# Kernel tuning notes

Hardware: AMD Instinct MI355X
Metric: run time of the kernel (lower is better)

## Reference

```python
import jax, jax.numpy as jnp
import numpy as np

B, L, C, D = 32, 256, 16, 128
WORD_VOCAB, CHR_VOCAB = 50000, 128


def conv1d(x, w, b):
    # x: [N, D, T], w: [D_out, D_in, 3], torch Conv1d (cross-correlation), padding=1
    y = jax.lax.conv_general_dilated(x, w, window_strides=(1,), padding=[(1, 1)],
                                     dimension_numbers=('NCH', 'OIH', 'NCH'))
    return y + b[None, :, None]


def setup_inputs() -> dict:
    key = jax.random.key(0)
    k1, k2, k3, k4, k5, k6, k7, k8 = jax.random.split(key, 8)
    word_vector = jax.random.randint(k1, (B, L), 0, WORD_VOCAB)
    words_in_char = jax.random.randint(k2, (B, L, C), 0, CHR_VOCAB)
    # embedding tables, padding_idx=0 -> row 0 is zeros
    word_table = (jax.random.normal(k3, (WORD_VOCAB, D), jnp.float32) * 0.02).at[0].set(0.0)
    chr_table = (jax.random.normal(k4, (CHR_VOCAB, D), jnp.float32) * 0.02).at[0].set(0.0)
    scale = 1.0 / np.sqrt(D * 3)
    conv_chr_w = jax.random.normal(k5, (D, D, 3), jnp.float32) * scale
    conv_chr_b = jax.random.normal(k6, (D,), jnp.float32) * scale
    conv_word_w = jax.random.normal(k7, (D, D, 3), jnp.float32) * scale
    conv_word_b = jax.random.normal(k8, (D,), jnp.float32) * scale
    return dict(word_vector=word_vector, words_in_char=words_in_char,
                word_table=word_table, chr_table=chr_table,
                conv_chr_w=conv_chr_w, conv_chr_b=conv_chr_b,
                conv_word_w=conv_word_w, conv_word_b=conv_word_b)


def reference(word_vector, words_in_char, word_table, chr_table,
              conv_chr_w, conv_chr_b, conv_word_w, conv_word_b):
    # --- char path (batched version of the per-word Python loop) ---
    chr_emb = chr_table[words_in_char]                       # [B, L, C, D]
    x = chr_emb.reshape(B * L, C, D).transpose(0, 2, 1)      # [B*L, D, C]
    word_conv = conv1d(x, conv_chr_w, conv_chr_b)            # [B*L, D, C]
    char_feats = word_conv.max(axis=2).reshape(B, L, D)      # max over char positions
    # --- word path ---
    word_emb = word_table[word_vector]                       # [B, L, D]
    out = conv1d(word_emb.transpose(0, 2, 1), conv_word_w, conv_word_b)  # [B, D, L]
    # stack both branch outputs into one array: [2, B, D, L]
    return jnp.stack([out, char_feats.transpose(0, 2, 1)])
```

## Files before the change

kernel.cpp:

```cpp
#include <hip/hip_runtime.h>

typedef __attribute__((ext_vector_type(8))) short short8;
typedef __attribute__((ext_vector_type(4))) float float4_t;

#define NB 32
#define NL 256
#define ND 128
#define OUT_PLANE (NB * ND * NL)
#define XS 136

__device__ inline unsigned short f2bf(float f) {
    union { float f; unsigned int i; } c;
    c.f = f;
    unsigned int r = c.i + 0x7FFFu + ((c.i >> 16) & 1u);
    return (unsigned short)(r >> 16);
}

__global__ void make_frags(const float* __restrict__ Wc,
                           const float* __restrict__ Ww,
                           unsigned short* __restrict__ out) {
    int i = blockIdx.x * 256 + threadIdx.x;
    const int half = 12 * 8 * 64 * 8;
    const float* W = (i < half) ? Wc : Ww;
    int ii = (i < half) ? i : i - half;
    int j    = ii & 7;
    int lane = (ii >> 3) & 63;
    int nt   = (ii >> 9) & 7;
    int s    = ii >> 12;
    int dout = nt * 16 + (lane & 15);
    int t    = s >> 2;
    int k    = (s & 3) * 32 + ((lane >> 4) & 3) * 8 + j;
    out[i] = f2bf(W[(dout * 128 + k) * 3 + t]);
}

__global__ __launch_bounds__(128, 2) void conv_kernel(
    const int* __restrict__ wv, const int* __restrict__ wic,
    const float* __restrict__ wordT, const float* __restrict__ chrT,
    const unsigned short* __restrict__ frags,
    const float* __restrict__ biasC, const float* __restrict__ biasW,
    float* __restrict__ out) {
    __shared__ unsigned short X[2][18 * XS];
    const int tid  = threadIdx.x;
    const int wave = tid >> 6, lane = tid & 63;
    const int m = lane & 15, quad = lane >> 4;
    const int bid = blockIdx.x;

    if (bid >= 512) {
        const int w0 = (bid - 512) * 8;
        short8 bfrag[12][4];
#pragma unroll
        for (int s = 0; s < 12; ++s)
#pragma unroll
            for (int p = 0; p < 4; ++p)
                bfrag[s][p] = *(const short8*)(
                    frags + (((s * 8 + wave * 4 + p) * 64 + lane) << 3));
        float bb[4];
#pragma unroll
        for (int p = 0; p < 4; ++p) bb[p] = biasC[wave * 64 + p * 16 + m];

        for (int p = tid; p < XS; p += 128) {
            X[0][p] = 0; X[0][17 * XS + p] = 0;
            X[1][p] = 0; X[1][17 * XS + p] = 0;
        }
        const int r = tid >> 3, seg = tid & 7;

        {
            int idx0 = wic[w0 * 16 + r];
            const float4_t* src = (const float4_t*)(chrT + idx0 * 128 + seg * 16);
            float4_t f0 = src[0], f1 = src[1], f2 = src[2], f3 = src[3];
            unsigned short t16[16];
            t16[0]=f2bf(f0.x); t16[1]=f2bf(f0.y); t16[2]=f2bf(f0.z); t16[3]=f2bf(f0.w);
            t16[4]=f2bf(f1.x); t16[5]=f2bf(f1.y); t16[6]=f2bf(f1.z); t16[7]=f2bf(f1.w);
            t16[8]=f2bf(f2.x); t16[9]=f2bf(f2.y); t16[10]=f2bf(f2.z); t16[11]=f2bf(f2.w);
            t16[12]=f2bf(f3.x); t16[13]=f2bf(f3.y); t16[14]=f2bf(f3.z); t16[15]=f2bf(f3.w);
            *(short8*)&X[0][(r + 1) * XS + seg * 16]     = *(const short8*)&t16[0];
            *(short8*)&X[0][(r + 1) * XS + seg * 16 + 8] = *(const short8*)&t16[8];
        }
        int idxA = wic[(w0 + 1) * 16 + r];
        __syncthreads();

#pragma unroll
        for (int wl = 0; wl < 8; ++wl) {
            const int cur = wl & 1;
            float4_t f0, f1, f2, f3;
            if (wl < 7) {
                const float4_t* src =
                    (const float4_t*)(chrT + idxA * 128 + seg * 16);
                f0 = src[0]; f1 = src[1]; f2 = src[2]; f3 = src[3];
            }
            int idxB = (wl < 6) ? wic[(w0 + wl + 2) * 16 + r] : 0;

            float4_t acc[4];
#pragma unroll
            for (int p = 0; p < 4; ++p) acc[p] = (float4_t){0.f, 0.f, 0.f, 0.f};
#pragma unroll
            for (int s = 0; s < 12; ++s) {
                short8 a = *(const short8*)&X[cur][(m + (s >> 2)) * XS +
                                                  (s & 3) * 32 + quad * 8];
#pragma unroll
                for (int p = 0; p < 4; ++p)
                    acc[p] = __builtin_amdgcn_mfma_f32_16x16x32_bf16(
                        a, bfrag[s][p], acc[p], 0, 0, 0);
            }

            if (wl < 7) {
                unsigned short t16[16];
                t16[0]=f2bf(f0.x); t16[1]=f2bf(f0.y); t16[2]=f2bf(f0.z); t16[3]=f2bf(f0.w);
                t16[4]=f2bf(f1.x); t16[5]=f2bf(f1.y); t16[6]=f2bf(f1.z); t16[7]=f2bf(f1.w);
                t16[8]=f2bf(f2.x); t16[9]=f2bf(f2.y); t16[10]=f2bf(f2.z); t16[11]=f2bf(f2.w);
                t16[12]=f2bf(f3.x); t16[13]=f2bf(f3.y); t16[14]=f2bf(f3.z); t16[15]=f2bf(f3.w);
                *(short8*)&X[cur ^ 1][(r + 1) * XS + seg * 16]     = *(const short8*)&t16[0];
                *(short8*)&X[cur ^ 1][(r + 1) * XS + seg * 16 + 8] = *(const short8*)&t16[8];
                idxA = idxB;
            }
            __syncthreads();

            int w = w0 + wl, b = w >> 8, l = w & 255;
            float* obase = out + OUT_PLANE + b * (ND * NL) + l;
#pragma unroll
            for (int p = 0; p < 4; ++p) {
                float v = fmaxf(fmaxf(acc[p].x, acc[p].y),
                                fmaxf(acc[p].z, acc[p].w));
                v = fmaxf(v, __shfl_xor(v, 16, 64));
                v = fmaxf(v, __shfl_xor(v, 32, 64));
                v += bb[p];
                if (quad == 0) obase[(wave * 64 + p * 16 + m) * NL] = v;
            }
        }
    } else {
        const int b = bid >> 4, l0 = (bid & 15) << 4;
        short8 bfrag[12][4];
#pragma unroll
        for (int s = 0; s < 12; ++s)
#pragma unroll
            for (int p = 0; p < 4; ++p)
                bfrag[s][p] = *(const short8*)(
                    frags + 49152 + (((s * 8 + wave * 4 + p) * 64 + lane) << 3));
        float bb[4];
#pragma unroll
        for (int p = 0; p < 4; ++p) bb[p] = biasW[wave * 64 + p * 16 + m];

#pragma unroll
        for (int i0 = 0; i0 < 2; ++i0) {
            int i = tid + i0 * 128;
            if (i < 144) {
                int rr = i >> 3, sg = i & 7;
                int l = l0 + rr - 1;
                int idx = (l >= 0 && l < NL) ? wv[b * NL + l] : 0;
                const float4_t* src =
                    (const float4_t*)(wordT + idx * 128 + sg * 16);
                float4_t f0 = src[0], f1 = src[1], f2 = src[2], f3 = src[3];
                unsigned short t16[16];
                t16[0]=f2bf(f0.x); t16[1]=f2bf(f0.y); t16[2]=f2bf(f0.z); t16[3]=f2bf(f0.w);
                t16[4]=f2bf(f1.x); t16[5]=f2bf(f1.y); t16[6]=f2bf(f1.z); t16[7]=f2bf(f1.w);
                t16[8]=f2bf(f2.x); t16[9]=f2bf(f2.y); t16[10]=f2bf(f2.z); t16[11]=f2bf(f2.w);
                t16[12]=f2bf(f3.x); t16[13]=f2bf(f3.y); t16[14]=f2bf(f3.z); t16[15]=f2bf(f3.w);
                *(short8*)&X[0][rr * XS + sg * 16]     = *(const short8*)&t16[0];
                *(short8*)&X[0][rr * XS + sg * 16 + 8] = *(const short8*)&t16[8];
            }
        }
        __syncthreads();

        float4_t acc[4];
#pragma unroll
        for (int p = 0; p < 4; ++p) acc[p] = (float4_t){0.f, 0.f, 0.f, 0.f};
#pragma unroll
        for (int s = 0; s < 12; ++s) {
            short8 a = *(const short8*)&X[0][(m + (s >> 2)) * XS +
                                            (s & 3) * 32 + quad * 8];
#pragma unroll
            for (int p = 0; p < 4; ++p)
                acc[p] = __builtin_amdgcn_mfma_f32_16x16x32_bf16(
                    a, bfrag[s][p], acc[p], 0, 0, 0);
        }

        float* obase = out + b * (ND * NL) + l0 + quad * 4;
#pragma unroll
        for (int p = 0; p < 4; ++p) {
            int dout = wave * 64 + p * 16 + m;
            float4_t pk;
            pk.x = acc[p].x + bb[p];
            pk.y = acc[p].y + bb[p];
            pk.z = acc[p].z + bb[p];
            pk.w = acc[p].w + bb[p];
            *(float4_t*)&obase[dout * NL] = pk;
        }
    }
}

extern "C" void kernel_launch(void* const* d_in, const int* in_sizes, int n_in,
                              void* d_out, int out_size, void* d_ws,
                              size_t ws_size, hipStream_t stream) {
    const int* word_vector   = (const int*)d_in[0];
    const int* words_in_char = (const int*)d_in[1];
    const float* word_table  = (const float*)d_in[2];
    const float* chr_table   = (const float*)d_in[3];
    const float* conv_chr_w  = (const float*)d_in[4];
    const float* conv_chr_b  = (const float*)d_in[5];
    const float* conv_word_w = (const float*)d_in[6];
    const float* conv_word_b = (const float*)d_in[7];
    float* out            = (float*)d_out;
    unsigned short* frags = (unsigned short*)d_ws;

    make_frags<<<384, 256, 0, stream>>>(conv_chr_w, conv_word_w, frags);
    conv_kernel<<<1536, 128, 0, stream>>>(word_vector, words_in_char,
                                          word_table, chr_table, frags,
                                          conv_chr_b, conv_word_b, out);
}
```

Baseline: 106.2 us.

## Preconvert char table to bf16 and load conv A-fragments directly from global

The prep kernel now also converts the 128x128 char embedding table to bf16 in the workspace. The char-path blocks then skip the LDS staging, double buffering and __syncthreads entirely: each lane gathers its shifted neighbour rows (m-1, m, m+1) as bf16 straight from global/L2 into registers, with zero padding at the word edges. This is meant to remove per-word LDS writes, f32-to-bf16 conversions and barriers. In exchange it adds more global gather loads per word, and the software prefetch is shallow, so load latency may be exposed.

```diff
diff --git a/kernel.cpp b/kernel.cpp
--- a/kernel.cpp
+++ b/kernel.cpp
@@ -8,6 +8,8 @@
 #define ND 128
 #define OUT_PLANE (NB * ND * NL)
 #define XS 136
+#define FR_WORD 49152
+#define CHRB 98304
 
 __device__ inline unsigned short f2bf(float f) {
     union { float f; unsigned int i; } c;
@@ -18,34 +20,40 @@
 
 __global__ void make_frags(const float* __restrict__ Wc,
                            const float* __restrict__ Ww,
+                           const float* __restrict__ chrT,
                            unsigned short* __restrict__ out) {
     int i = blockIdx.x * 256 + threadIdx.x;
-    const int half = 12 * 8 * 64 * 8;
-    const float* W = (i < half) ? Wc : Ww;
-    int ii = (i < half) ? i : i - half;
-    int j    = ii & 7;
-    int lane = (ii >> 3) & 63;
-    int nt   = (ii >> 9) & 7;
-    int s    = ii >> 12;
-    int dout = nt * 16 + (lane & 15);
-    int t    = s >> 2;
-    int k    = (s & 3) * 32 + ((lane >> 4) & 3) * 8 + j;
-    out[i] = f2bf(W[(dout * 128 + k) * 3 + t]);
+    if (i < CHRB) {
+        const float* W = (i < FR_WORD) ? Wc : Ww;
+        int ii = (i < FR_WORD) ? i : i - FR_WORD;
+        int j    = ii & 7;
+        int lane = (ii >> 3) & 63;
+        int nt   = (ii >> 9) & 7;
+        int s    = ii >> 12;
+        int dout = nt * 16 + (lane & 15);
+        int t    = s >> 2;
+        int k    = (s & 3) * 32 + ((lane >> 4) & 3) * 8 + j;
+        out[i] = f2bf(W[(dout * 128 + k) * 3 + t]);
+    } else {
+        int j = i - CHRB;
+        out[i] = f2bf(chrT[j]);
+    }
 }
 
 __global__ __launch_bounds__(128, 2) void conv_kernel(
     const int* __restrict__ wv, const int* __restrict__ wic,
-    const float* __restrict__ wordT, const float* __restrict__ chrT,
-    const unsigned short* __restrict__ frags,
+    const float* __restrict__ wordT,
+    const unsigned short* __restrict__ ws,
     const float* __restrict__ biasC, const float* __restrict__ biasW,
     float* __restrict__ out) {
-    __shared__ unsigned short X[2][18 * XS];
+    __shared__ unsigned short X[18 * XS];
     const int tid  = threadIdx.x;
     const int wave = tid >> 6, lane = tid & 63;
     const int m = lane & 15, quad = lane >> 4;
     const int bid = blockIdx.x;
 
     if (bid >= 512) {
+        const unsigned short* chrB = ws + CHRB;
         const int w0 = (bid - 512) * 8;
         short8 bfrag[12][4];
 #pragma unroll
@@ -53,69 +61,66 @@
 #pragma unroll
             for (int p = 0; p < 4; ++p)
                 bfrag[s][p] = *(const short8*)(
-                    frags + (((s * 8 + wave * 4 + p) * 64 + lane) << 3));
+                    ws + (((s * 8 + wave * 4 + p) * 64 + lane) << 3));
         float bb[4];
 #pragma unroll
         for (int p = 0; p < 4; ++p) bb[p] = biasC[wave * 64 + p * 16 + m];
 
-        for (int p = tid; p < XS; p += 128) {
-            X[0][p] = 0; X[0][17 * XS + p] = 0;
-            X[1][p] = 0; X[1][17 * XS + p] = 0;
-        }
-        const int r = tid >> 3, seg = tid & 7;
-
-        {
-            int idx0 = wic[w0 * 16 + r];
-            const float4_t* src = (const float4_t*)(chrT + idx0 * 128 + seg * 16);
-            float4_t f0 = src[0], f1 = src[1], f2 = src[2], f3 = src[3];
-            unsigned short t16[16];
-            t16[0]=f2bf(f0.x); t16[1]=f2bf(f0.y); t16[2]=f2bf(f0.z); t16[3]=f2bf(f0.w);
-            t16[4]=f2bf(f1.x); t16[5]=f2bf(f1.y); t16[6]=f2bf(f1.z); t16[7]=f2bf(f1.w);
-            t16[8]=f2bf(f2.x); t16[9]=f2bf(f2.y); t16[10]=f2bf(f2.z); t16[11]=f2bf(f2.w);
-            t16[12]=f2bf(f3.x); t16[13]=f2bf(f3.y); t16[14]=f2bf(f3.z); t16[15]=f2bf(f3.w);
-            *(short8*)&X[0][(r + 1) * XS + seg * 16]     = *(const short8*)&t16[0];
-            *(short8*)&X[0][(r + 1) * XS + seg * 16 + 8] = *(const short8*)&t16[8];
-        }
-        int idxA = wic[(w0 + 1) * 16 + r];
-        __syncthreads();
+        int base = w0 * 16 + m;
+        int i0 = (m >= 1)  ? wic[base - 1] : 0;
+        int i1 = wic[base];
+        int i2 = (m < 15) ? wic[base + 1] : 0;
 
 #pragma unroll
         for (int wl = 0; wl < 8; ++wl) {
-            const int cur = wl & 1;
-            float4_t f0, f1, f2, f3;
+            const int w = w0 + wl;
+            const unsigned short* r0 = chrB + i0 * 128 + (quad << 3);
+            const unsigned short* r1 = chrB + i1 * 128 + (quad << 3);
+            const unsigned short* r2 = chrB + i2 * 128 + (quad << 3);
+            short8 A[4];
+            A[0] = *(const short8*)(r0);
+            A[1] = *(const short8*)(r0 + 32);
+            A[2] = *(const short8*)(r0 + 64);
+            A[3] = *(const short8*)(r0 + 96);
+
             if (wl < 7) {
-                const float4_t* src =
-                    (const float4_t*)(chrT + idxA * 128 + seg * 16);
-                f0 = src[0]; f1 = src[1]; f2 = src[2]; f3 = src[3];
-            }
-            int idxB = (wl < 6) ? wic[(w0 + wl + 2) * 16 + r] : 0;
+                int nb = (w + 1) * 16 + m;
+                i0 = (m >= 1)  ? wic[nb - 1] : 0;
+                i1 = wic[nb];
+                i2 = (m < 15) ? wic[nb + 1] : 0;
+            }
 
             float4_t acc[4];
 #pragma unroll
             for (int p = 0; p < 4; ++p) acc[p] = (float4_t){0.f, 0.f, 0.f, 0.f};
-#pragma unroll
-            for (int s = 0; s < 12; ++s) {
-                short8 a = *(const short8*)&X[cur][(m + (s >> 2)) * XS +
-                                                  (s & 3) * 32 + quad * 8];
+
+#pragma unroll
+            for (int s = 0; s < 4; ++s) {
+                short8 a = A[s];
+                A[s] = *(const short8*)(r1 + (s << 5));
 #pragma unroll
                 for (int p = 0; p < 4; ++p)
                     acc[p] = __builtin_amdgcn_mfma_f32_16x16x32_bf16(
                         a, bfrag[s][p], acc[p], 0, 0, 0);
             }
-
-            if (wl < 7) {
-                unsigned short t16[16];
-                t16[0]=f2bf(f0.x); t16[1]=f2bf(f0.y); t16[2]=f2bf(f0.z); t16[3]=f2bf(f0.w);
-                t16[4]=f2bf(f1.x); t16[5]=f2bf(f1.y); t16[6]=f2bf(f1.z); t16[7]=f2bf(f1.w);
-                t16[8]=f2bf(f2.x); t16[9]=f2bf(f2.y); t16[10]=f2bf(f2.z); t16[11]=f2bf(f2.w);
-                t16[12]=f2bf(f3.x); t16[13]=f2bf(f3.y); t16[14]=f2bf(f3.z); t16[15]=f2bf(f3.w);
-                *(short8*)&X[cur ^ 1][(r + 1) * XS + seg * 16]     = *(const short8*)&t16[0];
-                *(short8*)&X[cur ^ 1][(r + 1) * XS + seg * 16 + 8] = *(const short8*)&t16[8];
-                idxA = idxB;
-            }
-            __syncthreads();
-
-            int w = w0 + wl, b = w >> 8, l = w & 255;
+#pragma unroll
+            for (int s = 0; s < 4; ++s) {
+                short8 a = A[s];
+                A[s] = *(const short8*)(r2 + (s << 5));
+#pragma unroll
+                for (int p = 0; p < 4; ++p)
+                    acc[p] = __builtin_amdgcn_mfma_f32_16x16x32_bf16(
+                        a, bfrag[s + 4][p], acc[p], 0, 0, 0);
+            }
+#pragma unroll
+            for (int s = 0; s < 4; ++s) {
+#pragma unroll
+                for (int p = 0; p < 4; ++p)
+                    acc[p] = __builtin_amdgcn_mfma_f32_16x16x32_bf16(
+                        A[s], bfrag[s + 8][p], acc[p], 0, 0, 0);
+            }
+
+            int b = w >> 8, l = w & 255;
             float* obase = out + OUT_PLANE + b * (ND * NL) + l;
 #pragma unroll
             for (int p = 0; p < 4; ++p) {
@@ -135,7 +140,7 @@
 #pragma unroll
             for (int p = 0; p < 4; ++p)
                 bfrag[s][p] = *(const short8*)(
-                    frags + 49152 + (((s * 8 + wave * 4 + p) * 64 + lane) << 3));
+                    ws + FR_WORD + (((s * 8 + wave * 4 + p) * 64 + lane) << 3));
         float bb[4];
 #pragma unroll
         for (int p = 0; p < 4; ++p) bb[p] = biasW[wave * 64 + p * 16 + m];
@@ -155,8 +160,8 @@
                 t16[4]=f2bf(f1.x); t16[5]=f2bf(f1.y); t16[6]=f2bf(f1.z); t16[7]=f2bf(f1.w);
                 t16[8]=f2bf(f2.x); t16[9]=f2bf(f2.y); t16[10]=f2bf(f2.z); t16[11]=f2bf(f2.w);
                 t16[12]=f2bf(f3.x); t16[13]=f2bf(f3.y); t16[14]=f2bf(f3.z); t16[15]=f2bf(f3.w);
-                *(short8*)&X[0][rr * XS + sg * 16]     = *(const short8*)&t16[0];
-                *(short8*)&X[0][rr * XS + sg * 16 + 8] = *(const short8*)&t16[8];
+                *(short8*)&X[rr * XS + sg * 16]     = *(const short8*)&t16[0];
+                *(short8*)&X[rr * XS + sg * 16 + 8] = *(const short8*)&t16[8];
             }
         }
         __syncthreads();
@@ -166,8 +171,8 @@
         for (int p = 0; p < 4; ++p) acc[p] = (float4_t){0.f, 0.f, 0.f, 0.f};
 #pragma unroll
         for (int s = 0; s < 12; ++s) {
-            short8 a = *(const short8*)&X[0][(m + (s >> 2)) * XS +
-                                            (s & 3) * 32 + quad * 8];
+            short8 a = *(const short8*)&X[(m + (s >> 2)) * XS +
+                                          (s & 3) * 32 + quad * 8];
 #pragma unroll
             for (int p = 0; p < 4; ++p)
                 acc[p] = __builtin_amdgcn_mfma_f32_16x16x32_bf16(
@@ -200,10 +205,10 @@
     const float* conv_word_w = (const float*)d_in[6];
     const float* conv_word_b = (const float*)d_in[7];
     float* out            = (float*)d_out;
-    unsigned short* frags = (unsigned short*)d_ws;
-
-    make_frags<<<384, 256, 0, stream>>>(conv_chr_w, conv_word_w, frags);
+    unsigned short* wsp   = (unsigned short*)d_ws;
+
+    make_frags<<<448, 256, 0, stream>>>(conv_chr_w, conv_word_w, chr_table, wsp);
     conv_kernel<<<1536, 128, 0, stream>>>(word_vector, words_in_char,
-                                          word_table, chr_table, frags,
+                                          word_table, wsp,
                                           conv_chr_b, conv_word_b, out);
 }
```

After: 117.8 us. +10.9%, slower.
